# Kernel tuning notes

Hardware: AMD Instinct MI355X
Metric: run time of the kernel (lower is better)

The kernel has to match this reference:

```python
import jax, jax.numpy as jnp
import numpy as np

N_NODES = 100000
N_EDGES = 600000
IN_C, HID_C, OUT_C = 128, 128, 64


def gcn_conv(x, W, b, src, dst, n_nodes):
    """PyG GCNConv: out = D^{-1/2} (A + I) D^{-1/2} X W + b (symmetric norm, self-loops)."""
    h = x @ W  # [N, C_out] transform first (as PyG does)
    # add self loops
    loop = jnp.arange(n_nodes, dtype=src.dtype)
    s = jnp.concatenate([src, loop])
    d = jnp.concatenate([dst, loop])
    # degree over targets (edge weight = 1)
    deg = jax.ops.segment_sum(jnp.ones_like(d, dtype=h.dtype), d, num_segments=n_nodes)
    dinv = jnp.where(deg > 0, jax.lax.rsqrt(deg), 0.0)
    norm = dinv[s] * dinv[d]  # [E+N]
    msg = h[s] * norm[:, None]  # gather + scale
    out = jax.ops.segment_sum(msg, d, num_segments=n_nodes)  # scatter-add
    return out + b


def setup_inputs() -> dict:
    key = jax.random.key(0)
    k1, k2, k3, k4, k5 = jax.random.split(key, 5)
    x = jax.random.normal(k1, (N_NODES, IN_C), dtype=jnp.float32)
    src = jax.random.randint(k2, (N_EDGES,), 0, N_NODES, dtype=jnp.int32)
    dst = jax.random.randint(k3, (N_EDGES,), 0, N_NODES, dtype=jnp.int32)
    # Glorot-style init for conv weights, zero bias (PyG defaults)
    W1 = jax.random.normal(k4, (IN_C, HID_C), dtype=jnp.float32) * (1.0 / np.sqrt(IN_C))
    W2 = jax.random.normal(k5, (HID_C, OUT_C), dtype=jnp.float32) * (1.0 / np.sqrt(HID_C))
    b1 = jnp.zeros((HID_C,), dtype=jnp.float32)
    b2 = jnp.zeros((OUT_C,), dtype=jnp.float32)
    return {"x": x, "W1": W1, "b1": b1, "W2": W2, "b2": b2, "src": src, "dst": dst}


def reference(x, W1, b1, W2, b2, src, dst):
    h = gcn_conv(x, W1, b1, src, dst, N_NODES)
    h = jax.nn.relu(h)
    out = gcn_conv(h, W2, b2, src, dst, N_NODES)
    return out
```

## Files before the change

### kernel.cpp

```cpp
#include <hip/hip_runtime.h>
#include <math.h>


typedef __bf16 bf16x8 __attribute__((ext_vector_type(8)));
typedef float f32x4 __attribute__((ext_vector_type(4)));

union ABu {
  unsigned short u16[8];
  uint4 u4;
  bf16x8 v;
};

__device__ inline unsigned short f2bf(float f) {
  unsigned u = __float_as_uint(f);
  return (unsigned short)((u + 0x7fffu + ((u >> 16) & 1u)) >> 16);
}

__device__ inline void unpack8(uint4 v, float* f) {
  f[0] = __uint_as_float(v.x << 16);
  f[1] = __uint_as_float(v.x & 0xffff0000u);
  f[2] = __uint_as_float(v.y << 16);
  f[3] = __uint_as_float(v.y & 0xffff0000u);
  f[4] = __uint_as_float(v.z << 16);
  f[5] = __uint_as_float(v.z & 0xffff0000u);
  f[6] = __uint_as_float(v.w << 16);
  f[7] = __uint_as_float(v.w & 0xffff0000u);
}

__device__ inline uint4 pack8(const float* a) {
  uint4 o;
  o.x = (unsigned)f2bf(a[0]) | ((unsigned)f2bf(a[1]) << 16);
  o.y = (unsigned)f2bf(a[2]) | ((unsigned)f2bf(a[3]) << 16);
  o.z = (unsigned)f2bf(a[4]) | ((unsigned)f2bf(a[5]) << 16);
  o.w = (unsigned)f2bf(a[6]) | ((unsigned)f2bf(a[7]) << 16);
  return o;
}

constexpr int SCAN_CHUNK = 1024;

__global__ __launch_bounds__(256) void k_pre(const float* __restrict__ W1,
                                             const float* __restrict__ W2,
                                             unsigned short* __restrict__ Wb1,
                                             unsigned short* __restrict__ Wb2,
                                             int* __restrict__ counts, int n) {
  constexpr int CONV_BLOCKS = (128 * 128 + 128 * 64) / 256;
  if (blockIdx.x < CONV_BLOCKS) {
    int idx = blockIdx.x * 256 + threadIdx.x;
    if (idx < 128 * 128) {
      int k = idx >> 7, c = idx & 127;
      Wb1[(((k >> 3) << 7) + c) * 8 + (k & 7)] = f2bf(W1[idx]);
    } else {
      int j = idx - 128 * 128;
      int k = j >> 6, c = j & 63;
      Wb2[(((k >> 3) << 6) + c) * 8 + (k & 7)] = f2bf(W2[j]);
    }
    return;
  }
  int i = (blockIdx.x - CONV_BLOCKS) * 256 + threadIdx.x;
  if (i < n) counts[i] = 0;
}

__global__ __launch_bounds__(256) void k_count_rank(const int* __restrict__ dst,
                                                    int* __restrict__ counts,
                                                    int* __restrict__ rank, int E) {
  int base = (blockIdx.x * 256 + threadIdx.x) * 4;
  if (base + 3 < E) {
    int4 d = *(const int4*)(dst + base);
    int4 r;
    r.x = atomicAdd(&counts[d.x], 1);
    r.y = atomicAdd(&counts[d.y], 1);
    r.z = atomicAdd(&counts[d.z], 1);
    r.w = atomicAdd(&counts[d.w], 1);
    *(int4*)(rank + base) = r;
  } else {
    for (int e = base; e < E; ++e) rank[e] = atomicAdd(&counts[dst[e]], 1);
  }
}

__global__ __launch_bounds__(256) void k_scan1(const int* __restrict__ counts,
                                               int* __restrict__ offsets,
                                               int* __restrict__ aux,
                                               float* __restrict__ dinv, int n) {
  __shared__ int tsum[256];
  int tid = threadIdx.x;
  int base = blockIdx.x * SCAN_CHUNK + tid * 4;
  int v0 = (base + 0 < n) ? counts[base + 0] : 0;
  int v1 = (base + 1 < n) ? counts[base + 1] : 0;
  int v2 = (base + 2 < n) ? counts[base + 2] : 0;
  int v3 = (base + 3 < n) ? counts[base + 3] : 0;
  int s = v0 + v1 + v2 + v3;
  tsum[tid] = s;
  __syncthreads();
  for (int off = 1; off < 256; off <<= 1) {
    int t = (tid >= off) ? tsum[tid - off] : 0;
    __syncthreads();
    tsum[tid] += t;
    __syncthreads();
  }
  int excl = tsum[tid] - s;
  if (base + 0 < n) { offsets[base + 0] = excl;              dinv[base + 0] = rsqrtf((float)(v0 + 1)); }
  if (base + 1 < n) { offsets[base + 1] = excl + v0;         dinv[base + 1] = rsqrtf((float)(v1 + 1)); }
  if (base + 2 < n) { offsets[base + 2] = excl + v0 + v1;    dinv[base + 2] = rsqrtf((float)(v2 + 1)); }
  if (base + 3 < n) { offsets[base + 3] = excl + v0 + v1 + v2; dinv[base + 3] = rsqrtf((float)(v3 + 1)); }
  if (tid == 255) aux[blockIdx.x] = tsum[255];
}

__global__ __launch_bounds__(256) void k_scan3(int* __restrict__ offsets,
                                               const int* __restrict__ aux,
                                               int n, int E, int G) {
  __shared__ int saux[256];
  int tid = threadIdx.x;
  int v = (tid < G) ? aux[tid] : 0;
  saux[tid] = v;
  __syncthreads();
  for (int off = 1; off < 256; off <<= 1) {
    int t = (tid >= off) ? saux[tid - off] : 0;
    __syncthreads();
    saux[tid] += t;
    __syncthreads();
  }
  int excl = saux[tid] - v;
  __syncthreads();
  saux[tid] = excl;
  __syncthreads();

  int i = blockIdx.x * 256 + tid;
  if (i < n) offsets[i] += saux[i >> 10];
  if (i == 0) offsets[n] = E;
}

__global__ __launch_bounds__(256) void k_scatter(const int* __restrict__ src,
                                                 const int* __restrict__ dst,
                                                 const int* __restrict__ offsets,
                                                 const int* __restrict__ rank,
                                                 int* __restrict__ esrc, int E) {
  int base = (blockIdx.x * 256 + threadIdx.x) * 4;
  if (base + 3 < E) {
    int4 s = *(const int4*)(src + base);
    int4 d = *(const int4*)(dst + base);
    int4 r = *(const int4*)(rank + base);
    esrc[offsets[d.x] + r.x] = s.x;
    esrc[offsets[d.y] + r.y] = s.y;
    esrc[offsets[d.z] + r.z] = s.z;
    esrc[offsets[d.w] + r.w] = s.w;
  } else {
    for (int e = base; e < E; ++e) esrc[offsets[dst[e]] + rank[e]] = src[e];
  }
}

__global__ __launch_bounds__(256) void k_gemm1(const float* __restrict__ X,
                                               const unsigned short* __restrict__ Wb,
                                               const float* __restrict__ dinv,
                                               unsigned short* __restrict__ Cb, int M) {
  constexpr int K = 128, N = 128, NT = N / 16, KS = K / 32;
  const int tid = threadIdx.x;
  const int wave = tid >> 6;
  const int lane = tid & 63;
  const int q = lane >> 4;
  const int l15 = lane & 15;
  const int row0 = blockIdx.x * 64 + wave * 16;
  const int rowA = row0 + l15;

  f32x4 zero = {0.0f, 0.0f, 0.0f, 0.0f};
  f32x4 acc[NT];
#pragma unroll
  for (int t = 0; t < NT; ++t) acc[t] = zero;

#pragma unroll
  for (int kk = 0; kk < KS; ++kk) {
    ABu a;
    float4 f0 = make_float4(0.f, 0.f, 0.f, 0.f);
    float4 f1 = make_float4(0.f, 0.f, 0.f, 0.f);
    if (rowA < M) {
      const float4* ap = (const float4*)(X + (size_t)rowA * K + kk * 32 + q * 8);
      f0 = ap[0];
      f1 = ap[1];
    }
    a.u16[0] = f2bf(f0.x); a.u16[1] = f2bf(f0.y);
    a.u16[2] = f2bf(f0.z); a.u16[3] = f2bf(f0.w);
    a.u16[4] = f2bf(f1.x); a.u16[5] = f2bf(f1.y);
    a.u16[6] = f2bf(f1.z); a.u16[7] = f2bf(f1.w);
#pragma unroll
    for (int nt = 0; nt < NT; ++nt) {
      ABu b;
      b.u4 = *(const uint4*)(Wb + ((size_t)(kk * 4 + q) * N + nt * 16 + l15) * 8);
      acc[nt] = __builtin_amdgcn_mfma_f32_16x16x32_bf16(a.v, b.v, acc[nt], 0, 0, 0);
    }
  }

#pragma unroll
  for (int v = 0; v < 4; ++v) {
    int row = row0 + q * 4 + v;
    if (row < M) {
      float di = dinv[row];
#pragma unroll
      for (int nt = 0; nt < NT; ++nt)
        Cb[(size_t)row * N + nt * 16 + l15] = f2bf(acc[nt][v] * di);
    }
  }
}

__global__ __launch_bounds__(256) void k_aggemm(const unsigned short* __restrict__ h1s,
                                                const float* __restrict__ dinv,
                                                const float* __restrict__ b1,
                                                const int* __restrict__ offsets,
                                                const int* __restrict__ esrc,
                                                const unsigned short* __restrict__ Wb2,
                                                unsigned short* __restrict__ h2s,
                                                int n) {
  constexpr int LDA = 136;
  __shared__ unsigned short As[16 * LDA];
  __shared__ float sdinv[16];
  const int tid = threadIdx.x;

  {
    const int nl = tid >> 4;
    const int q = tid & 15;
    const int node = blockIdx.x * 16 + nl;
    float acc[8];
    if (node < n) {
      const uint4* h4 = (const uint4*)h1s;
      float di = dinv[node];
      if (q == 0) sdinv[nl] = di;
      unpack8(h4[(size_t)node * 16 + q], acc);
      int e0 = offsets[node];
      int e1 = offsets[node + 1];
      for (int e = e0; e < e1; e += 8) {
        int idx[8];
#pragma unroll
        for (int i = 0; i < 8; ++i) {
          int ee = e + i < e1 ? e + i : e1 - 1;
          idx[i] = esrc[ee];
        }
        uint4 rr[8];
#pragma unroll
        for (int i = 0; i < 8; ++i) rr[i] = h4[(size_t)idx[i] * 16 + q];
#pragma unroll
        for (int i = 0; i < 8; ++i) {
          float w = (e + i < e1) ? 1.f : 0.f;
          float g[8];
          unpack8(rr[i], g);
#pragma unroll
          for (int j = 0; j < 8; ++j) acc[j] = fmaf(g[j], w, acc[j]);
        }
      }
      const float4* b14 = (const float4*)b1;
      float4 ba = b14[q * 2], bb = b14[q * 2 + 1];
      float bias[8] = {ba.x, ba.y, ba.z, ba.w, bb.x, bb.y, bb.z, bb.w};
#pragma unroll
      for (int i = 0; i < 8; ++i) acc[i] = fmaxf(fmaf(acc[i], di, bias[i]), 0.f);
    } else {
      if (q == 0) sdinv[nl] = 0.f;
#pragma unroll
      for (int i = 0; i < 8; ++i) acc[i] = 0.f;
    }
    *(uint4*)&As[nl * LDA + q * 8] = pack8(acc);
  }
  __syncthreads();

  {
    const int wave = tid >> 6;
    const int lane = tid & 63;
    const int q = lane >> 4;
    const int l15 = lane & 15;
    f32x4 acc = {0.0f, 0.0f, 0.0f, 0.0f};
#pragma unroll
    for (int kk = 0; kk < 4; ++kk) {
      ABu a, b;
      a.u4 = *(const uint4*)&As[l15 * LDA + kk * 32 + q * 8];
      b.u4 = *(const uint4*)(Wb2 + ((size_t)(kk * 4 + q) * 64 + wave * 16 + l15) * 8);
      acc = __builtin_amdgcn_mfma_f32_16x16x32_bf16(a.v, b.v, acc, 0, 0, 0);
    }
#pragma unroll
    for (int v = 0; v < 4; ++v) {
      int rl = q * 4 + v;
      int row = blockIdx.x * 16 + rl;
      if (row < n) h2s[(size_t)row * 64 + wave * 16 + l15] = f2bf(acc[v] * sdinv[rl]);
    }
  }
}

__global__ __launch_bounds__(256) void k_agg2(const unsigned short* __restrict__ h2s,
                                              const float* __restrict__ dinv,
                                              const float* __restrict__ b2,
                                              const int* __restrict__ offsets,
                                              const int* __restrict__ esrc,
                                              float* __restrict__ out, int n) {
  constexpr int CQ = 8;
  const int tid = threadIdx.x;
  const int node = blockIdx.x * 32 + tid / CQ;
  const int q = tid % CQ;
  if (node >= n) return;

  const uint4* h4 = (const uint4*)h2s;
  float di = dinv[node];
  float acc[8];
  unpack8(h4[(size_t)node * CQ + q], acc);

  int e0 = offsets[node];
  int e1 = offsets[node + 1];
  for (int e = e0; e < e1; e += 8) {
    int idx[8];
#pragma unroll
    for (int i = 0; i < 8; ++i) {
      int ee = e + i < e1 ? e + i : e1 - 1;
      idx[i] = esrc[ee];
    }
    uint4 rr[8];
#pragma unroll
    for (int i = 0; i < 8; ++i) rr[i] = h4[(size_t)idx[i] * CQ + q];
#pragma unroll
    for (int i = 0; i < 8; ++i) {
      float w = (e + i < e1) ? 1.f : 0.f;
      float g[8];
      unpack8(rr[i], g);
#pragma unroll
      for (int j = 0; j < 8; ++j) acc[j] = fmaf(g[j], w, acc[j]);
    }
  }

  const float4* b24 = (const float4*)b2;
  float4 ba = b24[q * 2], bb = b24[q * 2 + 1];
  float bias[8] = {ba.x, ba.y, ba.z, ba.w, bb.x, bb.y, bb.z, bb.w};
  float4 o0, o1;
  o0.x = fmaf(acc[0], di, bias[0]);
  o0.y = fmaf(acc[1], di, bias[1]);
  o0.z = fmaf(acc[2], di, bias[2]);
  o0.w = fmaf(acc[3], di, bias[3]);
  o1.x = fmaf(acc[4], di, bias[4]);
  o1.y = fmaf(acc[5], di, bias[5]);
  o1.z = fmaf(acc[6], di, bias[6]);
  o1.w = fmaf(acc[7], di, bias[7]);
  ((float4*)out)[(size_t)node * 16 + q * 2 + 0] = o0;
  ((float4*)out)[(size_t)node * 16 + q * 2 + 1] = o1;
}


extern "C" void kernel_launch(void* const* d_in, const int* in_sizes, int n_in,
                              void* d_out, int out_size, void* d_ws, size_t ws_size,
                              hipStream_t stream) {
  const float* x  = (const float*)d_in[0];
  const float* W1 = (const float*)d_in[1];
  const float* b1 = (const float*)d_in[2];
  const float* W2 = (const float*)d_in[3];
  const float* b2 = (const float*)d_in[4];
  const int* src  = (const int*)d_in[5];
  const int* dst  = (const int*)d_in[6];
  float* out = (float*)d_out;

  constexpr int IN_C = 128, HID_C = 128, OUT_C = 64;
  const int N = in_sizes[0] / IN_C;
  const int E = in_sizes[5];

  char* p = (char*)d_ws;
  auto alloc = [&](size_t bytes) {
    char* r = p;
    p += (bytes + 255) & ~(size_t)255;
    return r;
  };
  float* dinv    = (float*)alloc((size_t)N * 4);
  int*   offsets = (int*)alloc((size_t)(N + 1) * 4);
  int*   counts  = (int*)alloc((size_t)N * 4);
  int*   rank    = (int*)alloc((size_t)E * 4);
  int*   aux     = (int*)alloc(1024);
  int*   esrc    = (int*)alloc((size_t)E * 4);
  unsigned short* Wb1 = (unsigned short*)alloc((size_t)IN_C * HID_C * 2);
  unsigned short* Wb2 = (unsigned short*)alloc((size_t)HID_C * OUT_C * 2);
  unsigned short* h1s = (unsigned short*)alloc((size_t)N * HID_C * 2);
  unsigned short* h2s = (unsigned short*)alloc((size_t)N * OUT_C * 2);

  const int T = 256;
  const int G = (N + SCAN_CHUNK - 1) / SCAN_CHUNK;
  const int E4B = ((E + 3) / 4 + T - 1) / T;
  constexpr int CONV_BLOCKS = (128 * 128 + 128 * 64) / 256;

  k_pre<<<CONV_BLOCKS + (N + T - 1) / T, T, 0, stream>>>(W1, W2, Wb1, Wb2, counts, N);
  k_count_rank<<<E4B, T, 0, stream>>>(dst, counts, rank, E);
  k_scan1<<<G, T, 0, stream>>>(counts, offsets, aux, dinv, N);
  k_scan3<<<(N + T - 1) / T, T, 0, stream>>>(offsets, aux, N, E, G);
  k_scatter<<<E4B, T, 0, stream>>>(src, dst, offsets, rank, esrc, E);
  k_gemm1<<<(N + 63) / 64, T, 0, stream>>>(x, Wb1, dinv, h1s, N);
  k_aggemm<<<(N + 15) / 16, T, 0, stream>>>(h1s, dinv, b1, offsets, esrc, Wb2, h2s, N);
  k_agg2<<<(N + 31) / 32, T, 0, stream>>>(h2s, dinv, b2, offsets, esrc, out, N);
}
```

Measured before the change: 210.9 us.

## Split gemm1 across count and scatter launches, drop dinv prescale

Removes the dinv scaling from the first GEMM so it no longer depends on the degree scan. Its row blocks are split in two halves, fused into the count-rank and scatter launches as extra blocks so the GEMM overlaps with the atomic and scatter passes and one launch disappears. To compensate, the first aggregation now loads dinv of each neighbour per edge and scales gathered rows by it. That adds an extra random gather of dinv per edge.

```diff
diff --git a/kernel.cpp b/kernel.cpp
--- a/kernel.cpp
+++ b/kernel.cpp
@@ -60,10 +60,11 @@
   if (i < n) counts[i] = 0;
 }
 
-__global__ __launch_bounds__(256) void k_count_rank(const int* __restrict__ dst,
-                                                    int* __restrict__ counts,
-                                                    int* __restrict__ rank, int E) {
-  int base = (blockIdx.x * 256 + threadIdx.x) * 4;
+
+__device__ inline void count_body(const int* __restrict__ dst,
+                                  int* __restrict__ counts,
+                                  int* __restrict__ rank, int E, int bid) {
+  int base = (bid * 256 + (int)threadIdx.x) * 4;
   if (base + 3 < E) {
     int4 d = *(const int4*)(dst + base);
     int4 r;
@@ -75,6 +76,86 @@
   } else {
     for (int e = base; e < E; ++e) rank[e] = atomicAdd(&counts[dst[e]], 1);
   }
+}
+
+__device__ inline void scatter_body(const int* __restrict__ src,
+                                    const int* __restrict__ dst,
+                                    const int* __restrict__ offsets,
+                                    const int* __restrict__ rank,
+                                    int* __restrict__ esrc, int E, int bid) {
+  int base = (bid * 256 + (int)threadIdx.x) * 4;
+  if (base + 3 < E) {
+    int4 s = *(const int4*)(src + base);
+    int4 d = *(const int4*)(dst + base);
+    int4 r = *(const int4*)(rank + base);
+    esrc[offsets[d.x] + r.x] = s.x;
+    esrc[offsets[d.y] + r.y] = s.y;
+    esrc[offsets[d.z] + r.z] = s.z;
+    esrc[offsets[d.w] + r.w] = s.w;
+  } else {
+    for (int e = base; e < E; ++e) esrc[offsets[dst[e]] + rank[e]] = src[e];
+  }
+}
+
+__device__ inline void gemm1_body(const float* __restrict__ X,
+                                  const unsigned short* __restrict__ Wb,
+                                  unsigned short* __restrict__ Cb, int M,
+                                  int rowblk) {
+  constexpr int K = 128, N = 128, NT = N / 16, KS = K / 32;
+  const int tid = threadIdx.x;
+  const int wave = tid >> 6;
+  const int lane = tid & 63;
+  const int q = lane >> 4;
+  const int l15 = lane & 15;
+  const int row0 = rowblk * 64 + wave * 16;
+  const int rowA = row0 + l15;
+
+  f32x4 zero = {0.0f, 0.0f, 0.0f, 0.0f};
+  f32x4 acc[NT];
+#pragma unroll
+  for (int t = 0; t < NT; ++t) acc[t] = zero;
+
+#pragma unroll
+  for (int kk = 0; kk < KS; ++kk) {
+    ABu a;
+    float4 f0 = make_float4(0.f, 0.f, 0.f, 0.f);
+    float4 f1 = make_float4(0.f, 0.f, 0.f, 0.f);
+    if (rowA < M) {
+      const float4* ap = (const float4*)(X + (size_t)rowA * K + kk * 32 + q * 8);
+      f0 = ap[0];
+      f1 = ap[1];
+    }
+    a.u16[0] = f2bf(f0.x); a.u16[1] = f2bf(f0.y);
+    a.u16[2] = f2bf(f0.z); a.u16[3] = f2bf(f0.w);
+    a.u16[4] = f2bf(f1.x); a.u16[5] = f2bf(f1.y);
+    a.u16[6] = f2bf(f1.z); a.u16[7] = f2bf(f1.w);
+#pragma unroll
+    for (int nt = 0; nt < NT; ++nt) {
+      ABu b;
+      b.u4 = *(const uint4*)(Wb + ((size_t)(kk * 4 + q) * N + nt * 16 + l15) * 8);
+      acc[nt] = __builtin_amdgcn_mfma_f32_16x16x32_bf16(a.v, b.v, acc[nt], 0, 0, 0);
+    }
+  }
+
+#pragma unroll
+  for (int v = 0; v < 4; ++v) {
+    int row = row0 + q * 4 + v;
+    if (row < M) {
+#pragma unroll
+      for (int nt = 0; nt < NT; ++nt)
+        Cb[(size_t)row * N + nt * 16 + l15] = f2bf(acc[nt][v]);
+    }
+  }
+}
+
+__global__ __launch_bounds__(256) void k_count_gemm1(
+    const int* __restrict__ dst, int* __restrict__ counts, int* __restrict__ rank,
+    int E, int EB, const float* __restrict__ X,
+    const unsigned short* __restrict__ Wb1, unsigned short* __restrict__ h1, int M) {
+  if ((int)blockIdx.x < EB)
+    count_body(dst, counts, rank, E, blockIdx.x);
+  else
+    gemm1_body(X, Wb1, h1, M, blockIdx.x - EB);
 }
 
 __global__ __launch_bounds__(256) void k_scan1(const int* __restrict__ counts,
@@ -98,9 +179,9 @@
     __syncthreads();
   }
   int excl = tsum[tid] - s;
-  if (base + 0 < n) { offsets[base + 0] = excl;              dinv[base + 0] = rsqrtf((float)(v0 + 1)); }
-  if (base + 1 < n) { offsets[base + 1] = excl + v0;         dinv[base + 1] = rsqrtf((float)(v1 + 1)); }
-  if (base + 2 < n) { offsets[base + 2] = excl + v0 + v1;    dinv[base + 2] = rsqrtf((float)(v2 + 1)); }
+  if (base + 0 < n) { offsets[base + 0] = excl;                dinv[base + 0] = rsqrtf((float)(v0 + 1)); }
+  if (base + 1 < n) { offsets[base + 1] = excl + v0;           dinv[base + 1] = rsqrtf((float)(v1 + 1)); }
+  if (base + 2 < n) { offsets[base + 2] = excl + v0 + v1;      dinv[base + 2] = rsqrtf((float)(v2 + 1)); }
   if (base + 3 < n) { offsets[base + 3] = excl + v0 + v1 + v2; dinv[base + 3] = rsqrtf((float)(v3 + 1)); }
   if (tid == 255) aux[blockIdx.x] = tsum[255];
 }
@@ -129,78 +210,19 @@
   if (i == 0) offsets[n] = E;
 }
 
-__global__ __launch_bounds__(256) void k_scatter(const int* __restrict__ src,
-                                                 const int* __restrict__ dst,
-                                                 const int* __restrict__ offsets,
-                                                 const int* __restrict__ rank,
-                                                 int* __restrict__ esrc, int E) {
-  int base = (blockIdx.x * 256 + threadIdx.x) * 4;
-  if (base + 3 < E) {
-    int4 s = *(const int4*)(src + base);
-    int4 d = *(const int4*)(dst + base);
-    int4 r = *(const int4*)(rank + base);
-    esrc[offsets[d.x] + r.x] = s.x;
-    esrc[offsets[d.y] + r.y] = s.y;
-    esrc[offsets[d.z] + r.z] = s.z;
-    esrc[offsets[d.w] + r.w] = s.w;
-  } else {
-    for (int e = base; e < E; ++e) esrc[offsets[dst[e]] + rank[e]] = src[e];
-  }
-}
-
-__global__ __launch_bounds__(256) void k_gemm1(const float* __restrict__ X,
-                                               const unsigned short* __restrict__ Wb,
-                                               const float* __restrict__ dinv,
-                                               unsigned short* __restrict__ Cb, int M) {
-  constexpr int K = 128, N = 128, NT = N / 16, KS = K / 32;
-  const int tid = threadIdx.x;
-  const int wave = tid >> 6;
-  const int lane = tid & 63;
-  const int q = lane >> 4;
-  const int l15 = lane & 15;
-  const int row0 = blockIdx.x * 64 + wave * 16;
-  const int rowA = row0 + l15;
-
-  f32x4 zero = {0.0f, 0.0f, 0.0f, 0.0f};
-  f32x4 acc[NT];
-#pragma unroll
-  for (int t = 0; t < NT; ++t) acc[t] = zero;
-
-#pragma unroll
-  for (int kk = 0; kk < KS; ++kk) {
-    ABu a;
-    float4 f0 = make_float4(0.f, 0.f, 0.f, 0.f);
-    float4 f1 = make_float4(0.f, 0.f, 0.f, 0.f);
-    if (rowA < M) {
-      const float4* ap = (const float4*)(X + (size_t)rowA * K + kk * 32 + q * 8);
-      f0 = ap[0];
-      f1 = ap[1];
-    }
-    a.u16[0] = f2bf(f0.x); a.u16[1] = f2bf(f0.y);
-    a.u16[2] = f2bf(f0.z); a.u16[3] = f2bf(f0.w);
-    a.u16[4] = f2bf(f1.x); a.u16[5] = f2bf(f1.y);
-    a.u16[6] = f2bf(f1.z); a.u16[7] = f2bf(f1.w);
-#pragma unroll
-    for (int nt = 0; nt < NT; ++nt) {
-      ABu b;
-      b.u4 = *(const uint4*)(Wb + ((size_t)(kk * 4 + q) * N + nt * 16 + l15) * 8);
-      acc[nt] = __builtin_amdgcn_mfma_f32_16x16x32_bf16(a.v, b.v, acc[nt], 0, 0, 0);
-    }
-  }
-
-#pragma unroll
-  for (int v = 0; v < 4; ++v) {
-    int row = row0 + q * 4 + v;
-    if (row < M) {
-      float di = dinv[row];
-#pragma unroll
-      for (int nt = 0; nt < NT; ++nt)
-        Cb[(size_t)row * N + nt * 16 + l15] = f2bf(acc[nt][v] * di);
-    }
-  }
-}
-
-__global__ __launch_bounds__(256) void k_aggemm(const unsigned short* __restrict__ h1s,
+__global__ __launch_bounds__(256) void k_scatter_gemm1(
+    const int* __restrict__ src, const int* __restrict__ dst,
+    const int* __restrict__ offsets, const int* __restrict__ rank,
+    int* __restrict__ esrc, int E, int EB, const float* __restrict__ X,
+    const unsigned short* __restrict__ Wb1, unsigned short* __restrict__ h1,
+    int M, int rowblk0) {
+  if ((int)blockIdx.x < EB)
+    scatter_body(src, dst, offsets, rank, esrc, E, blockIdx.x);
+  else
+    gemm1_body(X, Wb1, h1, M, rowblk0 + (blockIdx.x - EB));
+}
+
+__global__ __launch_bounds__(256) void k_aggemm(const unsigned short* __restrict__ h1,
                                                 const float* __restrict__ dinv,
                                                 const float* __restrict__ b1,
                                                 const int* __restrict__ offsets,
@@ -219,10 +241,12 @@
     const int node = blockIdx.x * 16 + nl;
     float acc[8];
     if (node < n) {
-      const uint4* h4 = (const uint4*)h1s;
+      const uint4* h4 = (const uint4*)h1;
       float di = dinv[node];
       if (q == 0) sdinv[nl] = di;
       unpack8(h4[(size_t)node * 16 + q], acc);
+#pragma unroll
+      for (int j = 0; j < 8; ++j) acc[j] *= di;
       int e0 = offsets[node];
       int e1 = offsets[node + 1];
       for (int e = e0; e < e1; e += 8) {
@@ -232,16 +256,21 @@
           int ee = e + i < e1 ? e + i : e1 - 1;
           idx[i] = esrc[ee];
         }
+        float dv[8];
+#pragma unroll
+        for (int i = 0; i < 8; ++i) {
+          float dl = dinv[idx[i]];
+          dv[i] = (e + i < e1) ? dl : 0.f;
+        }
         uint4 rr[8];
 #pragma unroll
         for (int i = 0; i < 8; ++i) rr[i] = h4[(size_t)idx[i] * 16 + q];
 #pragma unroll
         for (int i = 0; i < 8; ++i) {
-          float w = (e + i < e1) ? 1.f : 0.f;
           float g[8];
           unpack8(rr[i], g);
 #pragma unroll
-          for (int j = 0; j < 8; ++j) acc[j] = fmaf(g[j], w, acc[j]);
+          for (int j = 0; j < 8; ++j) acc[j] = fmaf(g[j], dv[i], acc[j]);
         }
       }
       const float4* b14 = (const float4*)b1;
@@ -366,7 +395,7 @@
   int*   esrc    = (int*)alloc((size_t)E * 4);
   unsigned short* Wb1 = (unsigned short*)alloc((size_t)IN_C * HID_C * 2);
   unsigned short* Wb2 = (unsigned short*)alloc((size_t)HID_C * OUT_C * 2);
-  unsigned short* h1s = (unsigned short*)alloc((size_t)N * HID_C * 2);
+  unsigned short* h1  = (unsigned short*)alloc((size_t)N * HID_C * 2);
   unsigned short* h2s = (unsigned short*)alloc((size_t)N * OUT_C * 2);
 
   const int T = 256;
@@ -374,12 +403,16 @@
   const int E4B = ((E + 3) / 4 + T - 1) / T;
   constexpr int CONV_BLOCKS = (128 * 128 + 128 * 64) / 256;
 
+  const int RB_TOTAL = (N + 63) / 64;
+  const int RB_A = RB_TOTAL / 2;
+  const int RB_B = RB_TOTAL - RB_A;
+
   k_pre<<<CONV_BLOCKS + (N + T - 1) / T, T, 0, stream>>>(W1, W2, Wb1, Wb2, counts, N);
-  k_count_rank<<<E4B, T, 0, stream>>>(dst, counts, rank, E);
+  k_count_gemm1<<<E4B + RB_A, T, 0, stream>>>(dst, counts, rank, E, E4B, x, Wb1, h1, N);
   k_scan1<<<G, T, 0, stream>>>(counts, offsets, aux, dinv, N);
   k_scan3<<<(N + T - 1) / T, T, 0, stream>>>(offsets, aux, N, E, G);
-  k_scatter<<<E4B, T, 0, stream>>>(src, dst, offsets, rank, esrc, E);
-  k_gemm1<<<(N + 63) / 64, T, 0, stream>>>(x, Wb1, dinv, h1s, N);
-  k_aggemm<<<(N + 15) / 16, T, 0, stream>>>(h1s, dinv, b1, offsets, esrc, Wb2, h2s, N);
+  k_scatter_gemm1<<<E4B + RB_B, T, 0, stream>>>(src, dst, offsets, rank, esrc, E, E4B,
+                                                x, Wb1, h1, N, RB_A);
+  k_aggemm<<<(N + 15) / 16, T, 0, stream>>>(h1, dinv, b1, offsets, esrc, Wb2, h2s, N);
   k_agg2<<<(N + 31) / 32, T, 0, stream>>>(h2s, dinv, b2, offsets, esrc, out, N);
 }
```

After: 209.3 us. Within noise of the previous version (-0.7%).
